# Kernel tuning notes

Measured on AMD Instinct MI355X. Metric: run time of the kernel, lower is better.

The kernel has to match this reference:

```python
import jax, jax.numpy as jnp
import numpy as np

B, HW, N_L = 8, 5476, 32
DIM, L_IN, KC, VC, NH = 1024, 768, 1024, 1024, 8
EPS = 1e-5


def conv1(w, b, x):
    # 1x1 Conv1d == per-position linear. x: [B, C_in, L] -> [B, C_out, L]
    return jnp.einsum('oc,bcl->bol', w, x) + b[None, :, None]


def inorm(y):
    # InstanceNorm1d (affine=False): normalize each (batch, channel) over length.
    m = jnp.mean(y, axis=-1, keepdims=True)
    v = jnp.var(y, axis=-1, keepdims=True)
    return (y - m) * jax.lax.rsqrt(v + EPS)


def setup_inputs() -> dict:
    key = jax.random.key(0)
    ks = jax.random.split(key, 10)
    s = 0.02  # weight init scale
    x = jax.random.normal(ks[0], (B, HW, DIM), jnp.float32)
    l = jax.random.normal(ks[1], (B, N_L, L_IN), jnp.float32)
    l_mask = jax.random.randint(ks[2], (B, N_L, 1), 0, 2).astype(jnp.float32)
    l_mask = l_mask.at[:, 0, :].set(1.0)  # ensure at least one valid token
    return {
        'x': x, 'l': l, 'l_mask': l_mask,
        'vis_w': jax.random.normal(ks[3], (DIM, DIM), jnp.float32) * s,
        'vis_b': jnp.zeros((DIM,), jnp.float32),
        'fq_w': jax.random.normal(ks[4], (KC, DIM), jnp.float32) * s,
        'fq_b': jnp.zeros((KC,), jnp.float32),
        'fk_w': jax.random.normal(ks[5], (KC, L_IN), jnp.float32) * s,
        'fk_b': jnp.zeros((KC,), jnp.float32),
        'fv_w': jax.random.normal(ks[6], (VC, L_IN), jnp.float32) * s,
        'fv_b': jnp.zeros((VC,), jnp.float32),
        'W_w': jax.random.normal(ks[7], (VC, VC), jnp.float32) * s,
        'W_b': jnp.zeros((VC,), jnp.float32),
        'pm_w': jax.random.normal(ks[8], (VC, VC), jnp.float32) * s,
        'pm_b': jnp.zeros((VC,), jnp.float32),
    }


def reference(x, l, l_mask, vis_w, vis_b, fq_w, fq_b, fk_w, fk_b,
              fv_w, fv_b, W_w, W_b, pm_w, pm_b):
    # PWAM forward (eval mode, dropout=0)
    b, hw, _ = x.shape
    n_l = l.shape[1]
    xt = jnp.transpose(x, (0, 2, 1))            # [B, dim, HW]
    lt = jnp.transpose(l, (0, 2, 1))            # [B, l_in, N_l]
    mt = jnp.transpose(l_mask, (0, 2, 1))       # [B, 1, N_l]

    # vis_project: conv1d + GELU
    vis = jax.nn.gelu(conv1(vis_w, vis_b, xt), approximate=False)  # [B, dim, HW]

    # SpatialImageLanguageAttention
    q = inorm(conv1(fq_w, fq_b, xt))            # [B, KC, HW]
    k = conv1(fk_w, fk_b, lt) * mt              # [B, KC, N_l]
    v = conv1(fv_w, fv_b, lt) * mt              # [B, VC, N_l]

    qh = q.reshape(b, NH, KC // NH, hw).transpose(0, 1, 3, 2)  # [B, H, HW, dk]
    kh = k.reshape(b, NH, KC // NH, n_l)                       # [B, H, dk, N_l]
    vh = v.reshape(b, NH, VC // NH, n_l)                       # [B, H, dv, N_l]

    sim = jnp.einsum('bhqd,bhdk->bhqk', qh, kh) * (KC ** -0.5)
    sim = sim + (10000.0 * mt[:, None] - 10000.0)              # masked bias
    sim = jax.nn.softmax(sim, axis=-1)                          # [B, H, HW, N_l]

    out = jnp.einsum('bhqk,bhdk->bhqd', sim, vh)                # [B, H, HW, dv]
    out = out.transpose(0, 2, 1, 3).reshape(b, hw, VC)          # [B, HW, VC]
    out = jnp.transpose(out, (0, 2, 1))                         # [B, VC, HW]
    lang = inorm(conv1(W_w, W_b, out))                          # [B, VC, HW]

    # gated fusion + project_mm
    mm = vis * lang
    mm = jax.nn.gelu(conv1(pm_w, pm_b, mm), approximate=False)
    return jnp.transpose(mm, (0, 2, 1))                         # [B, HW, VC]
```

## Files before the change

kernel.cpp:

```cpp
#include <hip/hip_runtime.h>

typedef _Float16 f16;
typedef _Float16 f16x4 __attribute__((ext_vector_type(4)));
typedef _Float16 f16x8 __attribute__((ext_vector_type(8)));
typedef float f32x4 __attribute__((ext_vector_type(4)));

#define NB   8
#define HW   5476
#define NL   32
#define DIM  1024
#define LIN  768
#define MTOT (NB * HW)
#define MT256 ((MTOT + 255) / 256)
#define CSPLIT 128
#define ASPLIT 22


__device__ __forceinline__ void g2l16(const void* g, void* l) {
#if __has_builtin(__builtin_amdgcn_global_load_lds)
  __builtin_amdgcn_global_load_lds(
      (const __attribute__((address_space(1))) void*)g,
      (__attribute__((address_space(3))) void*)l, 16, 0, 0);
#else
  const int lane = threadIdx.x & 63;
  *(uint4*)((char*)l + lane * 16) = *(const uint4*)g;
#endif
}

__device__ __forceinline__ float gelu_f(float x) {
  return 0.5f * x * (1.0f + erff(x * 0.70710678118654752f));
}

#define WAITV(N) asm volatile("s_waitcnt vmcnt(" #N ")" ::: "memory")
__device__ __forceinline__ void barrier_nf() {
  asm volatile("s_barrier" ::: "memory");
}

__device__ __forceinline__ int swz32(int r, int q) {
  const int p = r >> 1;
  const int c = (((r & 1) << 2) | q) ^ (p & 7);
  return p * 64 + c * 8;
}

template <int EPI, int EPI2>
__global__ __launch_bounds__(512, 2) void gemm256(
    const f16* __restrict__ A, const f16* __restrict__ W,
    const float* __restrict__ bias, void* __restrict__ out,
    const f16* __restrict__ W2, const float* __restrict__ bias2,
    void* __restrict__ out2, int M) {
  constexpr int K = 1024, N = 1024;
  constexpr int KT = K / 32;
  constexpr int NT = (EPI2 >= 0) ? 8 : 4;
  constexpr int NWG = NT * MT256;
  constexpr int CHUNK = NWG / 8;
  __shared__ f16 lds[4][2][256 * 32];

  const int L = blockIdx.x;
  const int w = (L & 7) * CHUNK + (L >> 3);
  const int mt = w % MT256;
  int nt = w / MT256;
  const f16* Wp = W;
  const float* bp = bias;
  void* op = out;
  bool second = false;
  if constexpr (EPI2 >= 0) {
    if (nt >= 4) {
      nt -= 4;
      Wp = W2;
      bp = bias2;
      op = out2;
      second = true;
    }
  }

  const int tid = threadIdx.x;
  const int wave = tid >> 6, lane = tid & 63;
  const int m0 = mt * 256, n0 = nt * 256;
  const int wm = (wave >> 2) * 128;
  const int wn = (wave & 3) * 64;
  const int fr = lane & 15, fq = lane >> 4;

  f32x4 acc[8][4];
#pragma unroll
  for (int i = 0; i < 8; ++i)
#pragma unroll
    for (int j = 0; j < 4; ++j) acc[i][j] = (f32x4){0.f, 0.f, 0.f, 0.f};

  const int plocal = lane >> 3;
  const int csw = (lane & 7) ^ plocal;
  const int rofs = plocal * 2 + (csw >> 2);
  const int qofs = (csw & 3) * 8;

  auto stage = [&](int t) {
    const int buf = t & 3;
    const int k0 = t * 32;
    f16* Ab = &lds[buf][0][0];
    f16* Bb = &lds[buf][1][0];
#pragma unroll
    for (int la = 0; la < 2; ++la) {
      const int rg = wave * 2 + la;
      int gm = m0 + rg * 16 + rofs;
      if (gm > M - 1) gm = M - 1;
      g2l16(A + (size_t)gm * K + k0 + qofs, &Ab[rg * 512]);
    }
#pragma unroll
    for (int la = 0; la < 2; ++la) {
      const int rg = wave * 2 + la;
      const int gn = n0 + rg * 16 + rofs;
      g2l16(Wp + (size_t)gn * K + k0 + qofs, &Bb[rg * 512]);
    }
  };

  auto compute = [&](int t) {
    const f16* Ab = &lds[t & 3][0][0];
    const f16* Bb = &lds[t & 3][1][0];
    f16x8 af[8], bf[4];
#pragma unroll
    for (int i = 0; i < 8; ++i)
      af[i] = *(const f16x8*)&Ab[swz32(wm + i * 16 + fr, fq)];
#pragma unroll
    for (int j = 0; j < 4; ++j)
      bf[j] = *(const f16x8*)&Bb[swz32(wn + j * 16 + fr, fq)];
    __builtin_amdgcn_s_setprio(1);
#pragma unroll
    for (int i = 0; i < 8; ++i)
#pragma unroll
      for (int j = 0; j < 4; ++j)
        acc[i][j] = __builtin_amdgcn_mfma_f32_16x16x32_f16(af[i], bf[j],
                                                           acc[i][j], 0, 0, 0);
    __builtin_amdgcn_s_setprio(0);
  };

  stage(0);
  stage(1);
  stage(2);
#pragma unroll 4
  for (int t = 0; t < KT - 4; ++t) {
    WAITV(8);
    barrier_nf();
    stage(t + 3);
    compute(t);
  }
  WAITV(8); barrier_nf(); stage(KT - 1); compute(KT - 4);
  WAITV(8); barrier_nf(); compute(KT - 3);
  WAITV(4); barrier_nf(); compute(KT - 2);
  WAITV(0); barrier_nf(); compute(KT - 1);

  const bool do_gelu = second ? (EPI2 == 0 || EPI2 == 3) : (EPI == 0 || EPI == 3);
  const bool to_f16 = second ? (EPI2 <= 1) : (EPI <= 1);
  const int row0 = m0 + wm + fq * 4;
  const int col0 = n0 + wn + fr;
  float bv[4];
#pragma unroll
  for (int j = 0; j < 4; ++j) bv[j] = bp[col0 + j * 16];
#pragma unroll
  for (int i = 0; i < 8; ++i) {
#pragma unroll
    for (int r = 0; r < 4; ++r) {
      const int row = row0 + i * 16 + r;
      if (row < M) {
#pragma unroll
        for (int j = 0; j < 4; ++j) {
          float v = acc[i][j][r] + bv[j];
          if (do_gelu) v = gelu_f(v);
          if (to_f16)
            ((f16*)op)[(size_t)row * N + col0 + j * 16] = (f16)v;
          else
            ((float*)op)[(size_t)row * N + col0 + j * 16] = v;
        }
      }
    }
  }
}

__global__ void cvt_f32_f16(const float* __restrict__ in, f16* __restrict__ out,
                            int nchunks) {
  const int i = blockIdx.x * 256 + threadIdx.x;
  if (i >= nchunks) return;
  const float4* p = (const float4*)in + (size_t)i * 2;
  const float4 a = p[0], b = p[1];
  f16x8 o = {(f16)a.x, (f16)a.y, (f16)a.z, (f16)a.w,
             (f16)b.x, (f16)b.y, (f16)b.z, (f16)b.w};
  *((f16x8*)out + i) = o;
}

template <typename T>
__global__ __launch_bounds__(256) void colstats_partial(
    const T* __restrict__ X, float* __restrict__ psum,
    float* __restrict__ psq) {
  const int b = blockIdx.y;
  const int sp = blockIdx.x;
  const int c = threadIdx.x * 4;
  constexpr int CHUNK = (HW + CSPLIT - 1) / CSPLIT;
  const int r0 = sp * CHUNK;
  const int r1 = (r0 + CHUNK < HW) ? r0 + CHUNK : HW;

  float s0 = 0.f, s1 = 0.f, s2 = 0.f, s3 = 0.f;
  float q0 = 0.f, q1 = 0.f, q2 = 0.f, q3 = 0.f;
  const T* base = X + ((size_t)b * HW + r0) * DIM + c;
  for (int r = r0; r < r1; ++r) {
    float v0, v1, v2, v3;
    if constexpr (sizeof(T) == 2) {
      const f16x4 v = *(const f16x4*)base;
      v0 = (float)v[0]; v1 = (float)v[1]; v2 = (float)v[2]; v3 = (float)v[3];
    } else {
      const float4 v = *(const float4*)base;
      v0 = v.x; v1 = v.y; v2 = v.z; v3 = v.w;
    }
    s0 += v0; s1 += v1; s2 += v2; s3 += v3;
    q0 += v0 * v0; q1 += v1 * v1; q2 += v2 * v2; q3 += v3 * v3;
    base += DIM;
  }
  const size_t o = ((size_t)sp * NB + b) * DIM + c;
  *(float4*)&psum[o] = make_float4(s0, s1, s2, s3);
  *(float4*)&psq[o] = make_float4(q0, q1, q2, q3);
}

__global__ __launch_bounds__(256) void colstats_final(
    const float* __restrict__ psum, const float* __restrict__ psq,
    float* __restrict__ mean, float* __restrict__ rinv) {
  const int i = blockIdx.x * 256 + threadIdx.x;
  float s = 0.f, q = 0.f;
  for (int sp = 0; sp < CSPLIT; ++sp) {
    s += psum[(size_t)sp * NB * DIM + i];
    q += psq[(size_t)sp * NB * DIM + i];
  }
  const float m = s * (1.0f / HW);
  const float var = q * (1.0f / HW) - m * m;
  mean[i] = m;
  rinv[i] = rsqrtf(var + 1e-5f);
}

__global__ __launch_bounds__(256) void asum_final(
    const float* __restrict__ psum, float* __restrict__ mean) {
  const int i = blockIdx.x * 256 + threadIdx.x;
  float s = 0.f;
  for (int sp = 0; sp < ASPLIT; ++sp) s += psum[(size_t)sp * NB * DIM + i];
  mean[i] = s * (1.0f / HW);
}

__global__ __launch_bounds__(256) void kv_gemm(
    const float* __restrict__ l, const float* __restrict__ lmask,
    const float* __restrict__ wk, const float* __restrict__ bk,
    const float* __restrict__ wv, const float* __restrict__ bv,
    float* __restrict__ Kout, float* __restrict__ Vout) {
  const int b = blockIdx.z;
  const int o0 = blockIdx.x * 64;
  const float* w = blockIdx.y ? wv : wk;
  const float* bb = blockIdx.y ? bv : bk;
  float* out = blockIdx.y ? Vout : Kout;

  __shared__ float wl[64 * 129];
  __shared__ float ll[32 * 129];
  const int tid = threadIdx.x;
  const int o = tid & 63, ng = tid >> 6;
  float acc[8];
#pragma unroll
  for (int j = 0; j < 8; ++j) acc[j] = 0.f;

  for (int kc = 0; kc < LIN; kc += 128) {
    for (int e = tid; e < 64 * 128; e += 256)
      wl[(e >> 7) * 129 + (e & 127)] =
          w[(size_t)(o0 + (e >> 7)) * LIN + kc + (e & 127)];
    for (int e = tid; e < 32 * 128; e += 256)
      ll[(e >> 7) * 129 + (e & 127)] =
          l[(size_t)b * NL * LIN + (size_t)(e >> 7) * LIN + kc + (e & 127)];
    __syncthreads();
    for (int k = 0; k < 128; ++k) {
      const float wv_ = wl[o * 129 + k];
#pragma unroll
      for (int j = 0; j < 8; ++j) acc[j] += wv_ * ll[(ng * 8 + j) * 129 + k];
    }
    __syncthreads();
  }
  const float bval = bb[o0 + o];
#pragma unroll
  for (int j = 0; j < 8; ++j) {
    const int n = ng * 8 + j;
    out[((size_t)b * DIM + o0 + o) * NL + n] =
        (acc[j] + bval) * lmask[b * NL + n];
  }
}

__global__ __launch_bounds__(256) void attn_kernel(
    const f16* __restrict__ Q, const float* __restrict__ qmean,
    const float* __restrict__ qrinv, const float* __restrict__ Kk,
    const float* __restrict__ Vv, const float* __restrict__ lmask,
    float* __restrict__ Out, float* __restrict__ psum) {
  const int b = blockIdx.z, h = blockIdx.y;
  __shared__ float ks[128 * NL], vs[128 * NL], qm[128], qr[128], bs[NL];
  const int tid = threadIdx.x;
  const float* kbase = Kk + ((size_t)b * DIM + h * 128) * NL;
  const float* vbase = Vv + ((size_t)b * DIM + h * 128) * NL;
  for (int i = tid; i < 128 * NL; i += 256) {
    ks[i] = kbase[i];
    vs[i] = vbase[i];
  }
  if (tid < 128) {
    qm[tid] = qmean[b * DIM + h * 128 + tid];
    qr[tid] = qrinv[b * DIM + h * 128 + tid];
  }
  if (tid < NL) bs[tid] = (lmask[b * NL + tid] - 1.0f) * 10000.0f;
  __syncthreads();

  const int mloc = blockIdx.x * 256 + tid;
  const bool valid = mloc < HW;
  const int mc = valid ? mloc : HW - 1;
  const size_t m = (size_t)b * HW + mc;
  const f16* qrow = Q + m * DIM + h * 128;

  float sc[32];
#pragma unroll
  for (int n = 0; n < 32; ++n) sc[n] = 0.f;

  for (int d8 = 0; d8 < 16; ++d8) {
    const f16x8 qv = *(const f16x8*)(qrow + d8 * 8);
#pragma unroll
    for (int j = 0; j < 8; ++j) {
      const int d = d8 * 8 + j;
      const float qd = ((float)qv[j] - qm[d]) * qr[d];
      const float4* kr = (const float4*)&ks[d * 32];
#pragma unroll
      for (int n4 = 0; n4 < 8; ++n4) {
        const float4 kk = kr[n4];
        sc[n4 * 4 + 0] += qd * kk.x;
        sc[n4 * 4 + 1] += qd * kk.y;
        sc[n4 * 4 + 2] += qd * kk.z;
        sc[n4 * 4 + 3] += qd * kk.w;
      }
    }
  }
  float mx = -1e30f;
#pragma unroll
  for (int n = 0; n < 32; ++n) {
    sc[n] = sc[n] * 0.03125f + bs[n];
    mx = fmaxf(mx, sc[n]);
  }
  float sum = 0.f;
#pragma unroll
  for (int n = 0; n < 32; ++n) {
    sc[n] = __expf(sc[n] - mx);
    sum += sc[n];
  }
  const float rs = 1.0f / sum;

  float* orow = Out + m * DIM + h * 128;
  float* pbase = psum + ((size_t)blockIdx.x * NB + b) * DIM + h * 128;
  for (int dv8 = 0; dv8 < 16; ++dv8) {
    float ov[8];
#pragma unroll
    for (int j = 0; j < 8; ++j) {
      const float4* vr = (const float4*)&vs[(dv8 * 8 + j) * 32];
      float a = 0.f;
#pragma unroll
      for (int n4 = 0; n4 < 8; ++n4) {
        const float4 vv = vr[n4];
        a += sc[n4 * 4 + 0] * vv.x + sc[n4 * 4 + 1] * vv.y +
             sc[n4 * 4 + 2] * vv.z + sc[n4 * 4 + 3] * vv.w;
      }
      ov[j] = a * rs;
    }
    if (valid) {
      float4* op = (float4*)(orow + dv8 * 8);
      op[0] = make_float4(ov[0], ov[1], ov[2], ov[3]);
      op[1] = make_float4(ov[4], ov[5], ov[6], ov[7]);
    }
#pragma unroll
    for (int j = 0; j < 8; ++j) {
      float v = valid ? ov[j] : 0.f;
      v += __shfl_down(v, 32);
      v += __shfl_down(v, 16);
      v += __shfl_down(v, 8);
      v += __shfl_down(v, 4);
      v += __shfl_down(v, 2);
      v += __shfl_down(v, 1);
      if ((tid & 63) == 0) atomicAdd(&pbase[dv8 * 8 + j], v);
    }
  }
}

__global__ void center_kernel(const float* __restrict__ X,
                              const float* __restrict__ mean,
                              f16* __restrict__ out, int nchunks) {
  const int i = blockIdx.x * 256 + threadIdx.x;
  if (i >= nchunks) return;
  const size_t e = (size_t)i * 8;
  const int mrow = (int)(e >> 10);
  const int o = (int)(e & 1023);
  const int b = mrow / HW;
  const float4* p = (const float4*)(X + e);
  const float4 a = p[0], c = p[1];
  const float* mn = mean + b * DIM + o;
  f16x8 r = {(f16)(a.x - mn[0]), (f16)(a.y - mn[1]), (f16)(a.z - mn[2]),
             (f16)(a.w - mn[3]), (f16)(c.x - mn[4]), (f16)(c.y - mn[5]),
             (f16)(c.z - mn[6]), (f16)(c.w - mn[7])};
  *((f16x8*)out + i) = r;
}

__global__ void fuse_kernel(const f16* __restrict__ vis,
                            const float* __restrict__ lang,
                            const float* __restrict__ mean,
                            const float* __restrict__ rinv,
                            f16* __restrict__ out, int nchunks) {
  const int i = blockIdx.x * 256 + threadIdx.x;
  if (i >= nchunks) return;
  const size_t e = (size_t)i * 8;
  const int mrow = (int)(e >> 10);
  const int o = (int)(e & 1023);
  const int b = mrow / HW;
  const f16x8 v = *((const f16x8*)vis + i);
  const float4* p = (const float4*)(lang + e);
  const float4 a = p[0], c = p[1];
  const float lv[8] = {a.x, a.y, a.z, a.w, c.x, c.y, c.z, c.w};
  const float* mn = mean + b * DIM + o;
  const float* ri = rinv + b * DIM + o;
  f16x8 r;
#pragma unroll
  for (int j = 0; j < 8; ++j)
    r[j] = (f16)((float)v[j] * ((lv[j] - mn[j]) * ri[j]));
  *((f16x8*)out + i) = r;
}

extern "C" void kernel_launch(void* const* d_in, const int* in_sizes, int n_in,
                              void* d_out, int out_size, void* d_ws,
                              size_t ws_size, hipStream_t stream) {
  const float* x     = (const float*)d_in[0];
  const float* l     = (const float*)d_in[1];
  const float* lmask = (const float*)d_in[2];
  const float* vis_w = (const float*)d_in[3];
  const float* vis_b = (const float*)d_in[4];
  const float* fq_w  = (const float*)d_in[5];
  const float* fq_b  = (const float*)d_in[6];
  const float* fk_w  = (const float*)d_in[7];
  const float* fk_b  = (const float*)d_in[8];
  const float* fv_w  = (const float*)d_in[9];
  const float* fv_b  = (const float*)d_in[10];
  const float* W_w   = (const float*)d_in[11];
  const float* W_b   = (const float*)d_in[12];
  const float* pm_w  = (const float*)d_in[13];
  const float* pm_b  = (const float*)d_in[14];

  char* ws = (char*)d_ws;
  const size_t SB = (size_t)MTOT * DIM * 2;
  f16* Ah = (f16*)(ws);
  f16* Bh = (f16*)(ws + SB);
  f16* Ch = (f16*)(ws + 2 * SB);
  float* Df = (float*)(ws + 3 * SB);
  char* wsp = ws + 5 * SB;
  f16* vis_wh = (f16*)(wsp);
  f16* fq_wh  = (f16*)(wsp + (1 << 21));
  f16* W_wh   = (f16*)(wsp + 2 * (1 << 21));
  f16* pm_wh  = (f16*)(wsp + 3 * (1 << 21));
  float* Kout = (float*)(wsp + 4 * (1 << 21));
  float* Vout = (float*)(wsp + 4 * (1 << 21) + (1 << 20));
  float* st   = (float*)(wsp + 4 * (1 << 21) + 2 * (1 << 20));
  float* qmean = st;
  float* qrinv = st + 8192;
  float* amean = st + 16384;
  float* arinv = st + 24576;
  float* lmean = st + 32768;
  float* lrinv = st + 40960;
  float* psum  = (float*)(wsp + 4 * (1 << 21) + 3 * (1 << 20));
  float* psq   = psum + (size_t)CSPLIT * NB * DIM;

  const int NCH_BIG = MTOT * DIM / 8;
  const int NCH_W = DIM * DIM / 8;

  cvt_f32_f16<<<(NCH_BIG + 255) / 256, 256, 0, stream>>>(x, Ah, NCH_BIG);
  cvt_f32_f16<<<(NCH_W + 255) / 256, 256, 0, stream>>>(vis_w, vis_wh, NCH_W);
  cvt_f32_f16<<<(NCH_W + 255) / 256, 256, 0, stream>>>(fq_w, fq_wh, NCH_W);
  cvt_f32_f16<<<(NCH_W + 255) / 256, 256, 0, stream>>>(W_w, W_wh, NCH_W);
  cvt_f32_f16<<<(NCH_W + 255) / 256, 256, 0, stream>>>(pm_w, pm_wh, NCH_W);

  kv_gemm<<<dim3(16, 2, 8), 256, 0, stream>>>(l, lmask, fk_w, fk_b, fv_w, fv_b,
                                              Kout, Vout);

  gemm256<0, 1><<<8 * MT256, 512, 0, stream>>>(
      Ah, vis_wh, vis_b, Bh, fq_wh, fq_b, Ch, MTOT);

  colstats_partial<f16><<<dim3(CSPLIT, NB), 256, 0, stream>>>(Ch, psum, psq);
  colstats_final<<<32, 256, 0, stream>>>(psum, psq, qmean, qrinv);

  hipMemsetAsync(psum, 0, (size_t)ASPLIT * NB * DIM * sizeof(float), stream);
  attn_kernel<<<dim3((HW + 255) / 256, 8, 8), 256, 0, stream>>>(
      Ch, qmean, qrinv, Kout, Vout, lmask, Df, psum);
  asum_final<<<32, 256, 0, stream>>>(psum, amean);
  center_kernel<<<(NCH_BIG + 255) / 256, 256, 0, stream>>>(Df, amean, Ah,
                                                           NCH_BIG);

  gemm256<2, -1><<<4 * MT256, 512, 0, stream>>>(
      Ah, W_wh, W_b, Df, nullptr, nullptr, nullptr, MTOT);
  colstats_partial<float><<<dim3(CSPLIT, NB), 256, 0, stream>>>(Df, psum, psq);
  colstats_final<<<32, 256, 0, stream>>>(psum, psq, lmean, lrinv);
  fuse_kernel<<<(NCH_BIG + 255) / 256, 256, 0, stream>>>(Bh, Df, lmean, lrinv,
                                                         Ah, NCH_BIG);

  gemm256<3, -1><<<4 * MT256, 512, 0, stream>>>(
      Ah, pm_wh, pm_b, d_out, nullptr, nullptr, nullptr, MTOT);
}
```

Measured before the change: 1.474 ms.

## Fuse instance-norm statistics into GEMM epilogues and store intermediates in fp16

```diff
diff --git a/kernel.cpp b/kernel.cpp
--- a/kernel.cpp
+++ b/kernel.cpp
@@ -12,8 +12,6 @@
 #define LIN  768
 #define MTOT (NB * HW)
 #define MT256 ((MTOT + 255) / 256)
-#define CSPLIT 128
-#define ASPLIT 22
 
 
 __device__ __forceinline__ void g2l16(const void* g, void* l) {
@@ -42,12 +40,13 @@
   return p * 64 + c * 8;
 }
 
-template <int EPI, int EPI2>
+template <int EPI, int EPI2, int STATS>
 __global__ __launch_bounds__(512, 2) void gemm256(
     const f16* __restrict__ A, const f16* __restrict__ W,
     const float* __restrict__ bias, void* __restrict__ out,
     const f16* __restrict__ W2, const float* __restrict__ bias2,
-    void* __restrict__ out2, int M) {
+    void* __restrict__ out2, float* __restrict__ ssum,
+    float* __restrict__ ssq, int M) {
   constexpr int K = 1024, N = 1024;
   constexpr int KT = K / 32;
   constexpr int NT = (EPI2 >= 0) ? 8 : 4;
@@ -57,8 +56,8 @@
 
   const int L = blockIdx.x;
   const int w = (L & 7) * CHUNK + (L >> 3);
-  const int mt = w % MT256;
-  int nt = w / MT256;
+  const int mt = w / NT;
+  int nt = w % NT;
   const f16* Wp = W;
   const float* bp = bias;
   void* op = out;
@@ -148,11 +147,19 @@
 
   const bool do_gelu = second ? (EPI2 == 0 || EPI2 == 3) : (EPI == 0 || EPI == 3);
   const bool to_f16 = second ? (EPI2 <= 1) : (EPI <= 1);
+  const bool do_stats = (STATS == 2) || (STATS == 1 && second);
   const int row0 = m0 + wm + fq * 4;
   const int col0 = n0 + wn + fr;
   float bv[4];
 #pragma unroll
   for (int j = 0; j < 4; ++j) bv[j] = bp[col0 + j * 16];
+
+  const int bA = m0 / HW;
+  const int bnd = (bA + 1) * HW;
+  const bool straddle = (m0 + 255 >= bnd) && (bA + 1 < NB);
+  float sA[4] = {0, 0, 0, 0}, qA[4] = {0, 0, 0, 0};
+  float sB[4] = {0, 0, 0, 0}, qB[4] = {0, 0, 0, 0};
+
 #pragma unroll
   for (int i = 0; i < 8; ++i) {
 #pragma unroll
@@ -163,10 +170,43 @@
         for (int j = 0; j < 4; ++j) {
           float v = acc[i][j][r] + bv[j];
           if (do_gelu) v = gelu_f(v);
+          if constexpr (STATS != 0) {
+            if (do_stats) {
+              if (row < bnd) { sA[j] += v; qA[j] += v * v; }
+              else           { sB[j] += v; qB[j] += v * v; }
+            }
+          }
           if (to_f16)
             ((f16*)op)[(size_t)row * N + col0 + j * 16] = (f16)v;
           else
             ((float*)op)[(size_t)row * N + col0 + j * 16] = v;
+        }
+      }
+    }
+  }
+
+  if constexpr (STATS != 0) {
+    if (do_stats) {
+#pragma unroll
+      for (int j = 0; j < 4; ++j) {
+        float s = sA[j], q = qA[j];
+        s += __shfl_down(s, 16); s += __shfl_down(s, 32);
+        q += __shfl_down(q, 16); q += __shfl_down(q, 32);
+        if (lane < 16) {
+          atomicAdd(&ssum[(size_t)bA * DIM + col0 + j * 16], s);
+          atomicAdd(&ssq[(size_t)bA * DIM + col0 + j * 16], q);
+        }
+      }
+      if (straddle) {
+#pragma unroll
+        for (int j = 0; j < 4; ++j) {
+          float s = sB[j], q = qB[j];
+          s += __shfl_down(s, 16); s += __shfl_down(s, 32);
+          q += __shfl_down(q, 16); q += __shfl_down(q, 32);
+          if (lane < 16) {
+            atomicAdd(&ssum[(size_t)(bA + 1) * DIM + col0 + j * 16], s);
+            atomicAdd(&ssq[(size_t)(bA + 1) * DIM + col0 + j * 16], q);
+          }
         }
       }
     }
@@ -184,59 +224,19 @@
   *((f16x8*)out + i) = o;
 }
 
-template <typename T>
-__global__ __launch_bounds__(256) void colstats_partial(
-    const T* __restrict__ X, float* __restrict__ psum,
-    float* __restrict__ psq) {
-  const int b = blockIdx.y;
-  const int sp = blockIdx.x;
-  const int c = threadIdx.x * 4;
-  constexpr int CHUNK = (HW + CSPLIT - 1) / CSPLIT;
-  const int r0 = sp * CHUNK;
-  const int r1 = (r0 + CHUNK < HW) ? r0 + CHUNK : HW;
-
-  float s0 = 0.f, s1 = 0.f, s2 = 0.f, s3 = 0.f;
-  float q0 = 0.f, q1 = 0.f, q2 = 0.f, q3 = 0.f;
-  const T* base = X + ((size_t)b * HW + r0) * DIM + c;
-  for (int r = r0; r < r1; ++r) {
-    float v0, v1, v2, v3;
-    if constexpr (sizeof(T) == 2) {
-      const f16x4 v = *(const f16x4*)base;
-      v0 = (float)v[0]; v1 = (float)v[1]; v2 = (float)v[2]; v3 = (float)v[3];
-    } else {
-      const float4 v = *(const float4*)base;
-      v0 = v.x; v1 = v.y; v2 = v.z; v3 = v.w;
-    }
-    s0 += v0; s1 += v1; s2 += v2; s3 += v3;
-    q0 += v0 * v0; q1 += v1 * v1; q2 += v2 * v2; q3 += v3 * v3;
-    base += DIM;
-  }
-  const size_t o = ((size_t)sp * NB + b) * DIM + c;
-  *(float4*)&psum[o] = make_float4(s0, s1, s2, s3);
-  *(float4*)&psq[o] = make_float4(q0, q1, q2, q3);
-}
-
-__global__ __launch_bounds__(256) void colstats_final(
-    const float* __restrict__ psum, const float* __restrict__ psq,
+__global__ __launch_bounds__(256) void mean_rinv_final(
+    const float* __restrict__ sum, const float* __restrict__ sq,
     float* __restrict__ mean, float* __restrict__ rinv) {
   const int i = blockIdx.x * 256 + threadIdx.x;
-  float s = 0.f, q = 0.f;
-  for (int sp = 0; sp < CSPLIT; ++sp) {
-    s += psum[(size_t)sp * NB * DIM + i];
-    q += psq[(size_t)sp * NB * DIM + i];
-  }
-  const float m = s * (1.0f / HW);
-  const float var = q * (1.0f / HW) - m * m;
+  const float m = sum[i] * (1.0f / HW);
   mean[i] = m;
-  rinv[i] = rsqrtf(var + 1e-5f);
-}
-
-__global__ __launch_bounds__(256) void asum_final(
-    const float* __restrict__ psum, float* __restrict__ mean) {
+  rinv[i] = rsqrtf(sq[i] * (1.0f / HW) - m * m + 1e-5f);
+}
+
+__global__ __launch_bounds__(256) void mean_final(
+    const float* __restrict__ sum, float* __restrict__ mean) {
   const int i = blockIdx.x * 256 + threadIdx.x;
-  float s = 0.f;
-  for (int sp = 0; sp < ASPLIT; ++sp) s += psum[(size_t)sp * NB * DIM + i];
-  mean[i] = s * (1.0f / HW);
+  mean[i] = sum[i] * (1.0f / HW);
 }
 
 __global__ __launch_bounds__(256) void kv_gemm(
@@ -286,7 +286,7 @@
     const f16* __restrict__ Q, const float* __restrict__ qmean,
     const float* __restrict__ qrinv, const float* __restrict__ Kk,
     const float* __restrict__ Vv, const float* __restrict__ lmask,
-    float* __restrict__ Out, float* __restrict__ psum) {
+    f16* __restrict__ Out, float* __restrict__ asum) {
   const int b = blockIdx.z, h = blockIdx.y;
   __shared__ float ks[128 * NL], vs[128 * NL], qm[128], qr[128], bs[NL];
   const int tid = threadIdx.x;
@@ -344,8 +344,8 @@
   }
   const float rs = 1.0f / sum;
 
-  float* orow = Out + m * DIM + h * 128;
-  float* pbase = psum + ((size_t)blockIdx.x * NB + b) * DIM + h * 128;
+  f16* orow = Out + m * DIM + h * 128;
+  float* abase = asum + (size_t)b * DIM + h * 128;
   for (int dv8 = 0; dv8 < 16; ++dv8) {
     float ov[8];
 #pragma unroll
@@ -361,9 +361,9 @@
       ov[j] = a * rs;
     }
     if (valid) {
-      float4* op = (float4*)(orow + dv8 * 8);
-      op[0] = make_float4(ov[0], ov[1], ov[2], ov[3]);
-      op[1] = make_float4(ov[4], ov[5], ov[6], ov[7]);
+      f16x8 o = {(f16)ov[0], (f16)ov[1], (f16)ov[2], (f16)ov[3],
+                 (f16)ov[4], (f16)ov[5], (f16)ov[6], (f16)ov[7]};
+      *(f16x8*)(orow + dv8 * 8) = o;
     }
 #pragma unroll
     for (int j = 0; j < 8; ++j) {
@@ -374,12 +374,12 @@
       v += __shfl_down(v, 4);
       v += __shfl_down(v, 2);
       v += __shfl_down(v, 1);
-      if ((tid & 63) == 0) atomicAdd(&pbase[dv8 * 8 + j], v);
-    }
-  }
-}
-
-__global__ void center_kernel(const float* __restrict__ X,
+      if ((tid & 63) == 0) atomicAdd(&abase[dv8 * 8 + j], v);
+    }
+  }
+}
+
+__global__ void center_kernel(const f16* __restrict__ X,
                               const float* __restrict__ mean,
                               f16* __restrict__ out, int nchunks) {
   const int i = blockIdx.x * 256 + threadIdx.x;
@@ -388,17 +388,16 @@
   const int mrow = (int)(e >> 10);
   const int o = (int)(e & 1023);
   const int b = mrow / HW;
-  const float4* p = (const float4*)(X + e);
-  const float4 a = p[0], c = p[1];
+  const f16x8 v = *((const f16x8*)X + i);
   const float* mn = mean + b * DIM + o;
-  f16x8 r = {(f16)(a.x - mn[0]), (f16)(a.y - mn[1]), (f16)(a.z - mn[2]),
-             (f16)(a.w - mn[3]), (f16)(c.x - mn[4]), (f16)(c.y - mn[5]),
-             (f16)(c.z - mn[6]), (f16)(c.w - mn[7])};
+  f16x8 r;
+#pragma unroll
+  for (int j = 0; j < 8; ++j) r[j] = (f16)((float)v[j] - mn[j]);
   *((f16x8*)out + i) = r;
 }
 
 __global__ void fuse_kernel(const f16* __restrict__ vis,
-                            const float* __restrict__ lang,
+                            const f16* __restrict__ lang,
                             const float* __restrict__ mean,
                             const float* __restrict__ rinv,
                             f16* __restrict__ out, int nchunks) {
@@ -409,15 +408,13 @@
   const int o = (int)(e & 1023);
   const int b = mrow / HW;
   const f16x8 v = *((const f16x8*)vis + i);
-  const float4* p = (const float4*)(lang + e);
-  const float4 a = p[0], c = p[1];
-  const float lv[8] = {a.x, a.y, a.z, a.w, c.x, c.y, c.z, c.w};
+  const f16x8 lv = *((const f16x8*)lang + i);
   const float* mn = mean + b * DIM + o;
   const float* ri = rinv + b * DIM + o;
   f16x8 r;
 #pragma unroll
   for (int j = 0; j < 8; ++j)
-    r[j] = (f16)((float)v[j] * ((lv[j] - mn[j]) * ri[j]));
+    r[j] = (f16)((float)v[j] * (((float)lv[j] - mn[j]) * ri[j]));
   *((f16x8*)out + i) = r;
 }
 
@@ -442,10 +439,11 @@
 
   char* ws = (char*)d_ws;
   const size_t SB = (size_t)MTOT * DIM * 2;
-  f16* Ah = (f16*)(ws);
-  f16* Bh = (f16*)(ws + SB);
-  f16* Ch = (f16*)(ws + 2 * SB);
-  float* Df = (float*)(ws + 3 * SB);
+  f16* Ah  = (f16*)(ws);
+  f16* Bh  = (f16*)(ws + SB);
+  f16* Ch  = (f16*)(ws + 2 * SB);
+  f16* O16 = (f16*)(ws + 3 * SB);
+  f16* E16 = (f16*)(ws + 4 * SB);
   char* wsp = ws + 5 * SB;
   f16* vis_wh = (f16*)(wsp);
   f16* fq_wh  = (f16*)(wsp + (1 << 21));
@@ -457,14 +455,19 @@
   float* qmean = st;
   float* qrinv = st + 8192;
   float* amean = st + 16384;
-  float* arinv = st + 24576;
-  float* lmean = st + 32768;
-  float* lrinv = st + 40960;
-  float* psum  = (float*)(wsp + 4 * (1 << 21) + 3 * (1 << 20));
-  float* psq   = psum + (size_t)CSPLIT * NB * DIM;
+  float* lmean = st + 24576;
+  float* lrinv = st + 32768;
+  float* stats = (float*)(wsp + 4 * (1 << 21) + 3 * (1 << 20));
+  float* qsum = stats;
+  float* qsq  = stats + 8192;
+  float* asum = stats + 16384;
+  float* lsum = stats + 24576;
+  float* lsq  = stats + 32768;
 
   const int NCH_BIG = MTOT * DIM / 8;
   const int NCH_W = DIM * DIM / 8;
+
+  hipMemsetAsync(stats, 0, 5 * 8192 * sizeof(float), stream);
 
   cvt_f32_f16<<<(NCH_BIG + 255) / 256, 256, 0, stream>>>(x, Ah, NCH_BIG);
   cvt_f32_f16<<<(NCH_W + 255) / 256, 256, 0, stream>>>(vis_w, vis_wh, NCH_W);
@@ -475,26 +478,23 @@
   kv_gemm<<<dim3(16, 2, 8), 256, 0, stream>>>(l, lmask, fk_w, fk_b, fv_w, fv_b,
                                               Kout, Vout);
 
-  gemm256<0, 1><<<8 * MT256, 512, 0, stream>>>(
-      Ah, vis_wh, vis_b, Bh, fq_wh, fq_b, Ch, MTOT);
-
-  colstats_partial<f16><<<dim3(CSPLIT, NB), 256, 0, stream>>>(Ch, psum, psq);
-  colstats_final<<<32, 256, 0, stream>>>(psum, psq, qmean, qrinv);
-
-  hipMemsetAsync(psum, 0, (size_t)ASPLIT * NB * DIM * sizeof(float), stream);
+  gemm256<0, 1, 1><<<8 * MT256, 512, 0, stream>>>(
+      Ah, vis_wh, vis_b, Bh, fq_wh, fq_b, Ch, qsum, qsq, MTOT);
+  mean_rinv_final<<<32, 256, 0, stream>>>(qsum, qsq, qmean, qrinv);
+
   attn_kernel<<<dim3((HW + 255) / 256, 8, 8), 256, 0, stream>>>(
-      Ch, qmean, qrinv, Kout, Vout, lmask, Df, psum);
-  asum_final<<<32, 256, 0, stream>>>(psum, amean);
-  center_kernel<<<(NCH_BIG + 255) / 256, 256, 0, stream>>>(Df, amean, Ah,
+      Ch, qmean, qrinv, Kout, Vout, lmask, O16, asum);
+  mean_final<<<32, 256, 0, stream>>>(asum, amean);
+  center_kernel<<<(NCH_BIG + 255) / 256, 256, 0, stream>>>(O16, amean, Ah,
                                                            NCH_BIG);
 
-  gemm256<2, -1><<<4 * MT256, 512, 0, stream>>>(
-      Ah, W_wh, W_b, Df, nullptr, nullptr, nullptr, MTOT);
-  colstats_partial<float><<<dim3(CSPLIT, NB), 256, 0, stream>>>(Df, psum, psq);
-  colstats_final<<<32, 256, 0, stream>>>(psum, psq, lmean, lrinv);
-  fuse_kernel<<<(NCH_BIG + 255) / 256, 256, 0, stream>>>(Bh, Df, lmean, lrinv,
+  gemm256<1, -1, 2><<<4 * MT256, 512, 0, stream>>>(
+      Ah, W_wh, W_b, E16, nullptr, nullptr, nullptr, lsum, lsq, MTOT);
+  mean_rinv_final<<<32, 256, 0, stream>>>(lsum, lsq, lmean, lrinv);
+  fuse_kernel<<<(NCH_BIG + 255) / 256, 256, 0, stream>>>(Bh, E16, lmean, lrinv,
                                                          Ah, NCH_BIG);
 
-  gemm256<3, -1><<<4 * MT256, 512, 0, stream>>>(
-      Ah, pm_wh, pm_b, d_out, nullptr, nullptr, nullptr, MTOT);
-}
+  gemm256<3, -1, 0><<<4 * MT256, 512, 0, stream>>>(
+      Ah, pm_wh, pm_b, d_out, nullptr, nullptr, nullptr, nullptr, nullptr,
+      MTOT);
+}
```

Result: faster. 1.281 ms (-13.1%).
